# Kernel tuning notes

Hardware: AMD Instinct MI355X
Metric: run time of the kernel (lower is better)

The kernel has to match this reference:

```python
import jax, jax.numpy as jnp
import numpy as np
from jax import lax

N_NODES = 17
CONN = np.array([[15, 13], [13, 11], [16, 14], [14, 12], [11, 12], [5, 11], [6, 12],
                 [5, 6], [5, 7], [6, 8], [7, 9], [8, 10], [1, 2], [0, 1], [0, 2],
                 [1, 3], [2, 4], [3, 5], [4, 6]], dtype=np.int64)


def build_ahat():
    # PyG GCNConv norm: add self loops, deg = in-degree on target (col),
    # edge weight = deg^{-1/2}[src] * deg^{-1/2}[dst], aggregate src -> dst.
    src = np.concatenate([CONN[:, 0], np.arange(N_NODES)])
    dst = np.concatenate([CONN[:, 1], np.arange(N_NODES)])
    deg = np.zeros(N_NODES, dtype=np.float64)
    np.add.at(deg, dst, 1.0)
    dis = deg ** -0.5
    A = np.zeros((N_NODES, N_NODES), dtype=np.float64)
    np.add.at(A, (dst, src), dis[src] * dis[dst])
    return jnp.asarray(A, dtype=jnp.float32)

AHAT = build_ahat()  # (17, 17) normalized adjacency, directed as in source


def gcn_conv(h1, h2, W, b):
    # h1/h2: (B, T, 17, Cin). Only nodes 0..16 of the flattened cat(pose1, pose2)
    # batch -- i.e. pose1 sample 0 -- participate in message passing; all other
    # nodes only get their self-loop (weight 1) => plain linear.
    g1 = h1 @ W
    g2 = h2 @ W
    agg0 = jnp.einsum('ij,tjh->tih', AHAT, g1[0])  # (T, 17, H)
    g1 = g1.at[0].set(agg0)
    return g1 + b, g2 + b


def lstm_scan(x, Wih, Whh, bih, bhh, reverse=False):
    # x: (T, B, D). PyTorch gate order: i, f, g, o.
    B = x.shape[1]
    H = Whh.shape[1]
    xs = x[::-1] if reverse else x
    pre = xs @ Wih.T + (bih + bhh)  # (T, B, 4H), input part precomputed

    def step(carry, p):
        h, c = carry
        z = p + h @ Whh.T
        i, f, g, o = jnp.split(z, 4, axis=-1)
        c = jax.nn.sigmoid(f) * c + jax.nn.sigmoid(i) * jnp.tanh(g)
        h = jax.nn.sigmoid(o) * jnp.tanh(c)
        return (h, c), h

    init = (jnp.zeros((B, H), x.dtype), jnp.zeros((B, H), x.dtype))
    _, hs = lax.scan(step, init, pre)
    return hs[::-1] if reverse else hs  # time-ordered outputs (T, B, H)


def setup_inputs() -> dict:
    key = jax.random.key(0)
    ks = jax.random.split(key, 16)
    B, T, C_IN, H = 128, 256, 3, 128
    LH, NC = 256, 625
    D_LSTM = H * N_NODES  # 2176
    s = 0.05
    return {
        'pose1': jax.random.normal(ks[0], (B, T, N_NODES, C_IN), jnp.float32),
        'pose2': jax.random.normal(ks[1], (B, T, N_NODES, C_IN), jnp.float32),
        'W1': jax.random.normal(ks[2], (C_IN, H), jnp.float32) * s,
        'b1': jnp.zeros((H,), jnp.float32),
        'W2': jax.random.normal(ks[3], (H, H), jnp.float32) * s,
        'b2': jnp.zeros((H,), jnp.float32),
        'Wih_f': jax.random.normal(ks[4], (4 * LH, D_LSTM), jnp.float32) * s,
        'Whh_f': jax.random.normal(ks[5], (4 * LH, LH), jnp.float32) * s,
        'bih_f': jax.random.normal(ks[6], (4 * LH,), jnp.float32) * s,
        'bhh_f': jax.random.normal(ks[7], (4 * LH,), jnp.float32) * s,
        'Wih_b': jax.random.normal(ks[8], (4 * LH, D_LSTM), jnp.float32) * s,
        'Whh_b': jax.random.normal(ks[9], (4 * LH, LH), jnp.float32) * s,
        'bih_b': jax.random.normal(ks[10], (4 * LH,), jnp.float32) * s,
        'bhh_b': jax.random.normal(ks[11], (4 * LH,), jnp.float32) * s,
        'Wc': jax.random.normal(ks[12], (NC, 2 * LH), jnp.float32) * s,
        'bc': jnp.zeros((NC,), jnp.float32),
    }


def reference(pose1, pose2, W1, b1, W2, b2, Wih_f, Whh_f, bih_f, bhh_f,
              Wih_b, Whh_b, bih_b, bhh_b, Wc, bc):
    B, T = pose1.shape[:2]
    # GCN block (dropout is identity in eval mode)
    h1, h2 = gcn_conv(pose1, pose2, W1, b1)
    h1, h2 = jax.nn.relu(h1), jax.nn.relu(h2)
    h1, h2 = gcn_conv(h1, h2, W2, b2)
    # mean over the (pose1, pose2) pair, flatten node/channel dims
    feats = (0.5 * (h1 + h2)).reshape(B, T, -1)  # (B, T, 17*128)
    x = jnp.transpose(feats, (1, 0, 2))  # (T, B, D)
    hs_f = lstm_scan(x, Wih_f, Whh_f, bih_f, bhh_f, reverse=False)
    hs_b = lstm_scan(x, Wih_b, Whh_b, bih_b, bhh_b, reverse=True)
    last = jnp.concatenate([hs_f[-1], hs_b[-1]], axis=-1)  # (B, 512)
    feature_pool = jax.nn.relu(last)
    feature_cls = feature_pool @ Wc.T + bc
    return feature_pool, feature_cls
```

## Files before the change

### kernel.cpp

```cpp
#include <hip/hip_runtime.h>
#include <hip/hip_bf16.h>


#define TT 256
#define BB 128
#define NNODE 17
#define DD 2176
#define LHID 256
#define G4 1024
#define NCLS 625

typedef unsigned short u16t;

__device__ __constant__ int ESRC[19] = {15,13,16,14,11,5,6,5,5,6,7,8,1,0,0,1,2,3,4};
__device__ __constant__ int EDST[19] = {13,11,14,12,12,11,12,6,7,8,9,10,2,1,2,3,4,5,6};
__device__ __constant__ float DEGF[17] = {1,2,3,2,2,2,3,2,2,2,2,3,4,2,2,1,1};

__device__ inline float lo2f(unsigned u){ union{unsigned x; float f;} c; c.x = u << 16; return c.f; }
__device__ inline float hi2f(unsigned u){ union{unsigned x; float f;} c; c.x = u & 0xffff0000u; return c.f; }
__device__ inline u16t f2b(float f){
    __hip_bfloat16 h = __float2bfloat16(f);
    u16t s; __builtin_memcpy(&s, &h, 2); return s;
}
__device__ inline float b2f(u16t s){ union{unsigned x; float f;} c; c.x = ((unsigned)s) << 16; return c.f; }
__device__ inline unsigned pack2(float a, float b){
    return (unsigned)f2b(a) | ((unsigned)f2b(b) << 16);
}
__device__ inline float fsig(float x){ return __fdividef(1.f, 1.f + __expf(-x)); }
__device__ inline float ftanh(float x){ float e = __expf(2.f*x); return 1.f - __fdividef(2.f, e + 1.f); }
__device__ inline float sigm(float x){ return 1.f / (1.f + expf(-x)); }

typedef __attribute__((ext_vector_type(8))) short bf16x8;
typedef __attribute__((ext_vector_type(4))) float f32x4;
typedef __attribute__((ext_vector_type(4))) unsigned u32x4;

__device__ inline bf16x8 asB(u32x4 v){ bf16x8 r; __builtin_memcpy(&r, &v, 16); return r; }

__device__ inline void gload16(const void* g, void* l){
    __builtin_amdgcn_global_load_lds(
        (const __attribute__((address_space(1))) void*)g,
        (__attribute__((address_space(3))) void*)l, 16, 0, 0);
}

__global__ void k_w2t(const float* __restrict__ W2, __hip_bfloat16* __restrict__ W2Tb){
    int g = blockIdx.x * 256 + threadIdx.x;
    int k = g >> 7, n = g & 127;
    W2Tb[n * 128 + k] = __float2bfloat16(W2[g]);
}

__global__ void k_wb16(const float* __restrict__ W, u16t* __restrict__ Wb){
    int g = blockIdx.x * 256 + threadIdx.x;
    const float4 f0 = *(const float4*)(W + (size_t)g*8);
    const float4 f1 = *(const float4*)(W + (size_t)g*8 + 4);
    uint4 o;
    o.x = pack2(f0.x, f0.y); o.y = pack2(f0.z, f0.w);
    o.z = pack2(f1.x, f1.y); o.w = pack2(f1.z, f1.w);
    *(uint4*)(Wb + (size_t)g*8) = o;
}

__global__ void k_wfrag(const float* __restrict__ Whh, __hip_bfloat16* __restrict__ WTfrag){
    int g = blockIdx.x * 256 + threadIdx.x;
    int f = g >> 6, lane = g & 63;
    int w = f >> 5, kc = (f >> 2) & 7, nt = f & 3;
    int col = nt*256 + w*16 + (lane & 15);
    int k0  = kc*32 + (lane >> 4)*8;
    const float* src = Whh + (size_t)col * 256 + k0;
    float4 f0 = *(const float4*)src;
    float4 f1 = *(const float4*)(src + 4);
    uint4 o;
    o.x = pack2(f0.x, f0.y); o.y = pack2(f0.z, f0.w);
    o.z = pack2(f1.x, f1.y); o.w = pack2(f1.z, f1.w);
    *(uint4*)((char*)WTfrag + (size_t)g * 16) = o;
}

__global__ __launch_bounds__(512) void k_gcnfused(
    const float* __restrict__ pose1, const float* __restrict__ pose2,
    const float* __restrict__ W1, const float* __restrict__ b1,
    const float* __restrict__ b2, const __hip_bfloat16* __restrict__ W2Tb,
    __hip_bfloat16* __restrict__ feats)
{
    __shared__ u16t  Abuf[272][136];
    __shared__ u16t  BsmT[128][136];
    __shared__ float ps4[2][16][17][4];
    __shared__ float araw[17*128];
    __shared__ float araw2[17*128];
    __shared__ float As[289];

    const int tid = threadIdx.x;
    const int blk = blockIdx.x;
    const int t   = blk >> 3;
    const int bc  = blk & 7;

    for (int idx = tid; idx < 1632; idx += 512){
        int p_ = idx >= 816 ? 1 : 0;
        int r  = idx - p_ * 816;
        int bl = r / 51, i = r - bl * 51;
        int n = i / 3, c = i - n * 3;
        const float* src = p_ ? pose2 : pose1;
        ps4[p_][bl][n][c] = src[(size_t)((bc*16 + bl) * TT + t) * 51 + i];
    }
    {
        const uint4* src = (const uint4*)W2Tb;
        for (int r = 0; r < 2; ++r){
            int f0 = (tid + r * 512) * 16;
            int n = f0 >> 7, k0 = f0 & 127;
            uint4 v0 = src[(tid + r*512)*2 + 0];
            uint4 v1 = src[(tid + r*512)*2 + 1];
            *(uint4*)&BsmT[n][k0]     = v0;
            *(uint4*)&BsmT[n][k0 + 8] = v1;
        }
    }
    if (bc == 0 && tid < 289){
        int i = tid / 17, j = tid - (tid/17)*17;
        float a = (i == j) ? 1.0f / DEGF[i] : 0.0f;
        for (int e = 0; e < 19; ++e)
            if (EDST[e] == i && ESRC[e] == j)
                a += 1.0f / sqrtf(DEGF[i] * DEGF[j]);
        As[tid] = a;
    }

    const int h = tid & 127;
    const int q = tid >> 7;
    const float w10 = W1[h], w11 = W1[128 + h], w12 = W1[256 + h];
    const float b1h = b1[h];
    __syncthreads();

    float a2st[5];
    int nl[5], nv = 0;
    for (int s = 0; s < 5; ++s){ int n = q + 4*s; if (n < NNODE) nl[nv++] = n; }
    for (int s = 0; s < nv; ++s){
        int n = nl[s];
        for (int bl = 0; bl < 16; ++bl){
            float4 p1 = *(const float4*)&ps4[0][bl][n][0];
            float4 p2 = *(const float4*)&ps4[1][bl][n][0];
            float a1 = p1.x*w10 + p1.y*w11 + p1.z*w12;
            float a2 = p2.x*w10 + p2.y*w11 + p2.z*w12;
            if (bc == 0 && bl == 0){
                araw[n*128 + h] = a1;
                a2st[s] = a2;
            } else {
                float r1 = fmaxf(a1 + b1h, 0.f);
                float r2 = fmaxf(a2 + b1h, 0.f);
                Abuf[n*16 + bl][h] = f2b(0.5f*(r1 + r2));
            }
        }
    }
    __syncthreads();
    if (bc == 0){
        for (int s = 0; s < nv; ++s){
            int n = nl[s]; float a = 0.f;
            #pragma unroll
            for (int j = 0; j < NNODE; ++j) a += As[n*17 + j] * araw[j*128 + h];
            araw2[n*128 + h] = fmaxf(a + b1h, 0.f);
        }
    }
    __syncthreads();
    if (bc == 0){
        for (int s = 0; s < nv; ++s){
            int n = nl[s]; float a = 0.f;
            #pragma unroll
            for (int j = 0; j < NNODE; ++j) a += As[n*17 + j] * araw2[j*128 + h];
            float r2 = fmaxf(a2st[s] + b1h, 0.f);
            Abuf[n*16 + 0][h] = f2b(0.5f*(a + r2));
        }
    }
    __syncthreads();

    const int w = tid >> 6, l = tid & 63;
    const int l15 = l & 15, q8 = (l >> 4) * 8, q4 = (l >> 4) * 4;
    float bias[8];
    #pragma unroll
    for (int nt = 0; nt < 8; ++nt) bias[nt] = b2[nt*16 + l15];

    bf16x8 Bf[4][8];
    #pragma unroll
    for (int kc = 0; kc < 4; ++kc)
        #pragma unroll
        for (int nt = 0; nt < 8; ++nt)
            Bf[kc][nt] = *(const bf16x8*)&BsmT[nt*16 + l15][kc*32 + q8];

    u16t* Cb = (u16t*)feats;
    for (int mt = w; mt < NNODE; mt += 8){
        f32x4 acc[8];
        #pragma unroll
        for (int nt = 0; nt < 8; ++nt) acc[nt] = (f32x4){0.f,0.f,0.f,0.f};
        #pragma unroll
        for (int kc = 0; kc < 4; ++kc){
            bf16x8 a = *(const bf16x8*)&Abuf[mt*16 + l15][kc*32 + q8];
            #pragma unroll
            for (int nt = 0; nt < 8; ++nt)
                acc[nt] = __builtin_amdgcn_mfma_f32_16x16x32_bf16(a, Bf[kc][nt], acc[nt], 0,0,0);
        }
        #pragma unroll
        for (int nt = 0; nt < 8; ++nt)
            #pragma unroll
            for (int r = 0; r < 4; ++r){
                size_t row = (size_t)(blk*16 + q4 + r) * NNODE + mt;
                Cb[row*128 + nt*16 + l15] = f2b(acc[nt][r] + bias[nt]);
            }
    }
}

__global__ __launch_bounds__(256) void k_gemm_mfma(
    const __hip_bfloat16* __restrict__ A, const float* __restrict__ Bw,
    const u16t* __restrict__ Bb,
    const float* __restrict__ bi1, const float* __restrict__ bi2,
    u16t* __restrict__ pre2)
{
    __shared__ u16t Asm[128][32];
    __shared__ u16t Bsm[128][32];
    const int tid = threadIdx.x;
    const int w = tid >> 6;
    const int l = tid & 63;

    const int blk = blockIdx.x;
    const int xcd = blk & 7;
    const int i_  = blk >> 3;
    const int bx  = xcd * 32 + (i_ >> 3);
    const int by  = i_ & 7;

    const size_t m0 = (size_t)bx * 128;
    const int n0 = by * 128;
    const int mw = (w >> 1) * 64;
    const int nw = (w & 1) * 64;

    f32x4 acc[4][4];
    #pragma unroll
    for (int s = 0; s < 4; ++s)
        #pragma unroll
        for (int t_ = 0; t_ < 4; ++t_)
            acc[s][t_] = (f32x4){0.f, 0.f, 0.f, 0.f};

    const u16t* Ab = (const u16t*)A;
    const int arow = w*32 + (l>>2);
    const int akoff = (l&3)*8;
    const int brow = w*32 + (l>>1);
    const int bko  = (l&1)*16;
    const int fr = l & 15, fq = (l >> 4) * 8;

    for (int kt = 0; kt < DD; kt += 32){
        gload16(Ab + (m0 + arow)*DD + kt + akoff,      &Asm[arow][akoff]);
        gload16(Ab + (m0 + arow + 16)*DD + kt + akoff, &Asm[arow+16][akoff]);
        if (Bb){
            gload16(Bb + (size_t)(n0 + arow)*DD + kt + akoff,      &Bsm[arow][akoff]);
            gload16(Bb + (size_t)(n0 + arow + 16)*DD + kt + akoff, &Bsm[arow+16][akoff]);
        } else {
            const float* bp = Bw + (size_t)(n0 + brow)*DD + kt + bko;
            float4 f0 = *(const float4*)bp;
            float4 f1 = *(const float4*)(bp+4);
            float4 f2 = *(const float4*)(bp+8);
            float4 f3 = *(const float4*)(bp+12);
            uint4 o0, o1;
            o0.x = pack2(f0.x,f0.y); o0.y = pack2(f0.z,f0.w);
            o0.z = pack2(f1.x,f1.y); o0.w = pack2(f1.z,f1.w);
            o1.x = pack2(f2.x,f2.y); o1.y = pack2(f2.z,f2.w);
            o1.z = pack2(f3.x,f3.y); o1.w = pack2(f3.z,f3.w);
            *(uint4*)&Bsm[brow][bko]   = o0;
            *(uint4*)&Bsm[brow][bko+8] = o1;
        }
        __syncthreads();

        bf16x8 af[4], bf[4];
        #pragma unroll
        for (int s = 0; s < 4; ++s) af[s] = *(const bf16x8*)&Asm[mw + s*16 + fr][fq];
        #pragma unroll
        for (int t_ = 0; t_ < 4; ++t_) bf[t_] = *(const bf16x8*)&Bsm[nw + t_*16 + fr][fq];
        #pragma unroll
        for (int s = 0; s < 4; ++s)
            #pragma unroll
            for (int t_ = 0; t_ < 4; ++t_)
                acc[s][t_] = __builtin_amdgcn_mfma_f32_16x16x32_bf16(af[s], bf[t_], acc[s][t_], 0, 0, 0);
        __syncthreads();
    }

    const int cr = (l >> 4) * 4;
    const int cc = l & 15;
    const int tIdx = bx;
    #pragma unroll
    for (int t_ = 0; t_ < 4; ++t_){
        int col = n0 + nw + t_*16 + cc;
        float bias = bi1[col] + bi2[col];
        int gate = col >> 8;
        int j    = col & 255;
        size_t cbase = (size_t)tIdx*131072 + (size_t)(j>>4)*1024 + (size_t)(j&15)*4 + gate;
        #pragma unroll
        for (int s = 0; s < 4; ++s)
            #pragma unroll
            for (int r = 0; r < 4; ++r){
                int b = mw + s*16 + cr + r;
                pre2[cbase + (size_t)(b>>4)*16384 + ((b&15)>>2)*256 + (b&3)*64]
                    = f2b(acc[s][t_][r] + bias);
            }
    }
}

__global__ __launch_bounds__(256) void k_lstm_b(
    const __hip_bfloat16* __restrict__ feats255,
    const float* __restrict__ Wih_b,
    const float* __restrict__ bih_b, const float* __restrict__ bhh_b,
    float* __restrict__ h_b)
{
    __shared__ float fs[DD];
    const int tid = threadIdx.x;
    const int b = blockIdx.x;
    const unsigned* fbu = (const unsigned*)(feats255 + (size_t)b * DD);
    for (int i = tid; i < DD/2; i += 256){
        unsigned u = fbu[i];
        fs[2*i] = lo2f(u); fs[2*i+1] = hi2f(u);
    }
    __syncthreads();

    const int w = tid >> 6, lane = tid & 63;
    const int j = blockIdx.y * 4 + w;
    const float* Wi = Wih_b + (size_t)j * DD;
    const float* Wg = Wih_b + (size_t)(512 + j) * DD;
    const float* Wo = Wih_b + (size_t)(768 + j) * DD;
    float si = 0.f, sg = 0.f, so = 0.f;
    #pragma unroll 2
    for (int i = 0; i < 34; ++i){
        int k = lane + i*64;
        float f = fs[k];
        si += f * Wi[k]; sg += f * Wg[k]; so += f * Wo[k];
    }
    #pragma unroll
    for (int off = 32; off > 0; off >>= 1){
        si += __shfl_down(si, off);
        sg += __shfl_down(sg, off);
        so += __shfl_down(so, off);
    }
    if (lane == 0){
        float zi = si + bih_b[j]       + bhh_b[j];
        float zg = sg + bih_b[512 + j] + bhh_b[512 + j];
        float zo = so + bih_b[768 + j] + bhh_b[768 + j];
        float c = sigm(zi) * tanhf(zg);
        h_b[(size_t)b*LHID + j] = sigm(zo) * tanhf(c);
    }
}

__global__ __launch_bounds__(1024, 4) void k_lstm_f11(
    const u16t* __restrict__ pre2,
    const __hip_bfloat16* __restrict__ WTfrag,
    float* __restrict__ hout)
{
    __shared__ u16t Wl[65536];
    __shared__ __align__(16) float zbuf[256][4];
    __shared__ __align__(16) u16t hbuf[256];

    const int tid = threadIdx.x;
    const int w = tid >> 6, l = tid & 63;
    const int q = l >> 4, l15 = l & 15, q8 = q * 8;
    const int g = blockIdx.x;
    const u16t* wtf = (const u16t*)WTfrag;

    {
        const uint4* srcq = (const uint4*)wtf;
        uint4* dstq = (uint4*)Wl;
        for (int i = tid; i < 8192; i += 1024){
            int iw = i >> 9, fi = (i >> 6) & 7, il = i & 63;
            dstq[i] = srcq[(iw*32 + 24 + fi)*64 + il];
        }
    }
    if (tid < 256) hbuf[tid] = 0;

    u32x4 Bv[6][4];
    #pragma unroll
    for (int kc = 0; kc < 6; ++kc)
        #pragma unroll
        for (int nt = 0; nt < 4; ++nt){
            Bv[kc][nt] = *(const u32x4*)(wtf + (((size_t)(w*32 + kc*4 + nt))*64 + l)*8);
            asm volatile("" : "+v"(Bv[kc][nt]));
        }

    const int j = tid;
    float cst = 0.f;
    const size_t pj = (size_t)(g >> 4)*16384 + (size_t)((g & 15) >> 2)*256
                    + (size_t)(g & 3)*64 + (size_t)(j >> 4)*1024 + (size_t)(j & 15)*4;
    const u16t* pp = pre2 + pj;
    union { uint2 v; u16t s4[4]; } prc, prn;
    if (tid < 256) prc.v = *(const uint2*)pp;
    __syncthreads();

    #pragma unroll 1
    for (int t = 0; t < TT; ++t){
        if (tid < 256){
            int tn = (t + 1 < TT) ? t + 1 : t;
            prn.v = *(const uint2*)(pp + (size_t)tn*131072);
        }

        f32x4 acc[4];
        #pragma unroll
        for (int nt = 0; nt < 4; ++nt) acc[nt] = (f32x4){0.f,0.f,0.f,0.f};

        #pragma unroll
        for (int kc = 6; kc < 8; ++kc){
            bf16x8 ah = *(const bf16x8*)&hbuf[kc*32 + q8];
            #pragma unroll
            for (int nt = 0; nt < 4; ++nt){
                bf16x8 bL = *(const bf16x8*)&Wl[((w*8 + (kc-6)*4 + nt)*64 + l)*8];
                acc[nt] = __builtin_amdgcn_mfma_f32_16x16x32_bf16(ah, bL, acc[nt], 0,0,0);
            }
        }
        #pragma unroll
        for (int kc = 0; kc < 6; ++kc){
            bf16x8 ah = *(const bf16x8*)&hbuf[kc*32 + q8];
            #pragma unroll
            for (int nt = 0; nt < 4; ++nt)
                acc[nt] = __builtin_amdgcn_mfma_f32_16x16x32_bf16(ah, asB(Bv[kc][nt]), acc[nt], 0,0,0);
        }

        if (q == 0){
            float4 zq;
            zq.x = acc[0][0]; zq.y = acc[1][0]; zq.z = acc[2][0]; zq.w = acc[3][0];
            *(float4*)&zbuf[w*16 + l15][0] = zq;
        }
        __syncthreads();

        if (tid < 256){
            float4 z = *(const float4*)&zbuf[j][0];
            float zi = z.x + b2f(prc.s4[0]);
            float zf = z.y + b2f(prc.s4[1]);
            float zg = z.z + b2f(prc.s4[2]);
            float zo = z.w + b2f(prc.s4[3]);
            float cn = fsig(zf)*cst + fsig(zi)*ftanh(zg);
            cst = cn;
            float hh = fsig(zo)*ftanh(cn);
            if (t < TT - 1)
                hbuf[j] = f2b(hh);
            else
                hout[(size_t)g*LHID + j] = hh;
        }
        prc = prn;
        __syncthreads();
    }
}

__global__ __launch_bounds__(256) void k_head(
    const float* __restrict__ h_f, const float* __restrict__ h_b,
    const float* __restrict__ Wc, const float* __restrict__ bc,
    float* __restrict__ out)
{
    __shared__ float pool[512];
    const int b = blockIdx.x, tid = threadIdx.x;
    float p0 = fmaxf(h_f[(size_t)b*LHID + tid], 0.f);
    float p1 = fmaxf(h_b[(size_t)b*LHID + tid], 0.f);
    pool[tid] = p0; pool[256 + tid] = p1;
    out[(size_t)b*512 + tid]       = p0;
    out[(size_t)b*512 + 256 + tid] = p1;
    __syncthreads();
    for (int n = tid; n < NCLS; n += 256){
        float a = bc[n];
        const float* ww = Wc + (size_t)n * 512;
        #pragma unroll 4
        for (int k = 0; k < 512; k += 4){
            float4 wv = *(const float4*)(ww + k);
            a += pool[k]*wv.x + pool[k+1]*wv.y + pool[k+2]*wv.z + pool[k+3]*wv.w;
        }
        out[(size_t)BB*512 + (size_t)b*NCLS + n] = a;
    }
}

extern "C" void kernel_launch(void* const* d_in, const int* in_sizes, int n_in,
                              void* d_out, int out_size, void* d_ws, size_t ws_size,
                              hipStream_t stream) {
    const float* pose1 = (const float*)d_in[0];
    const float* pose2 = (const float*)d_in[1];
    const float* W1    = (const float*)d_in[2];
    const float* b1    = (const float*)d_in[3];
    const float* W2    = (const float*)d_in[4];
    const float* b2    = (const float*)d_in[5];
    const float* Wih_f = (const float*)d_in[6];
    const float* Whh_f = (const float*)d_in[7];
    const float* bih_f = (const float*)d_in[8];
    const float* bhh_f = (const float*)d_in[9];
    const float* Wih_b = (const float*)d_in[10];
    const float* bih_b = (const float*)d_in[12];
    const float* bhh_b = (const float*)d_in[13];
    const float* Wc    = (const float*)d_in[14];
    const float* bc    = (const float*)d_in[15];
    (void)in_sizes; (void)n_in; (void)out_size;
    float* out = (float*)d_out;
    char* ws = (char*)d_ws;

    __hip_bfloat16* WTfrag = (__hip_bfloat16*)(ws + 0);
    __hip_bfloat16* W2Tb   = (__hip_bfloat16*)(ws + 524288);
    float*          h_b    = (float*)(ws + 557056);
    float*          h_f    = (float*)(ws + 688128);
    __hip_bfloat16* feats  = (__hip_bfloat16*)(ws + 2097152);
    u16t*           pre2   = (u16t*)(ws + 144703488);

    const size_t BASE = 211812352, WBSZ = 4456448;
    const bool haveWb = (ws_size >= BASE + WBSZ);
    u16t* Wb16 = haveWb ? (u16t*)(ws + BASE) : (u16t*)nullptr;

    k_w2t     <<<64, 256, 0, stream>>>(W2, W2Tb);
    k_wfrag   <<<128, 256, 0, stream>>>(Whh_f, WTfrag);
    if (haveWb)
        k_wb16<<<1088, 256, 0, stream>>>(Wih_f, Wb16);
    k_gcnfused<<<2048, 512, 0, stream>>>(pose1, pose2, W1, b1, b2, W2Tb, feats);
    k_gemm_mfma<<<2048, 256, 0, stream>>>(feats, Wih_f, Wb16, bih_f, bhh_f, pre2);
    k_lstm_b  <<<dim3(128, 64), 256, 0, stream>>>(feats + (size_t)255*BB*DD, Wih_b, bih_b, bhh_b, h_b);
    k_lstm_f11<<<128, 1024, 0, stream>>>(pre2, WTfrag, h_f);
    k_head    <<<128, 256, 0, stream>>>(h_f, h_b, Wc, bc, out);
}
```

Baseline: 1.029 ms.

## Halve LSTM recurrence block to 512 threads, two tiles per wave in AGPRs

The forward LSTM recurrent kernel now runs with 512 threads instead of 1024, and each wave computes two 16-column gate tiles instead of one. The register-resident Whh fragments double and are pinned to accumulation registers (AGPRs) via an inline-asm constraint. Fewer waves means a cheaper per-step __syncthreads barrier and more MFMA work per wave between barriers. The cost is higher register pressure and less latency hiding per step.

```diff
diff --git a/kernel.cpp b/kernel.cpp
--- a/kernel.cpp
+++ b/kernel.cpp
@@ -337,7 +337,7 @@
     }
 }
 
-__global__ __launch_bounds__(1024, 4) void k_lstm_f11(
+__global__ __launch_bounds__(512, 2) void k_lstm_f16(
     const u16t* __restrict__ pre2,
     const __hip_bfloat16* __restrict__ WTfrag,
     float* __restrict__ hout)
@@ -355,21 +355,25 @@
     {
         const uint4* srcq = (const uint4*)wtf;
         uint4* dstq = (uint4*)Wl;
-        for (int i = tid; i < 8192; i += 1024){
+        for (int i = tid; i < 8192; i += 512){
             int iw = i >> 9, fi = (i >> 6) & 7, il = i & 63;
             dstq[i] = srcq[(iw*32 + 24 + fi)*64 + il];
         }
     }
     if (tid < 256) hbuf[tid] = 0;
 
-    u32x4 Bv[6][4];
+    u32x4 Ba[2][6][4];
     #pragma unroll
-    for (int kc = 0; kc < 6; ++kc)
-        #pragma unroll
-        for (int nt = 0; nt < 4; ++nt){
-            Bv[kc][nt] = *(const u32x4*)(wtf + (((size_t)(w*32 + kc*4 + nt))*64 + l)*8);
-            asm volatile("" : "+v"(Bv[kc][nt]));
-        }
+    for (int s = 0; s < 2; ++s){
+        const int wt = w + s*8;
+        #pragma unroll
+        for (int kc = 0; kc < 6; ++kc)
+            #pragma unroll
+            for (int nt = 0; nt < 4; ++nt){
+                Ba[s][kc][nt] = *(const u32x4*)(wtf + (((size_t)(wt*32 + kc*4 + nt))*64 + l)*8);
+                asm volatile("" : "+a"(Ba[s][kc][nt]));
+            }
+    }
 
     const int j = tid;
     float cst = 0.f;
@@ -387,31 +391,41 @@
             prn.v = *(const uint2*)(pp + (size_t)tn*131072);
         }
 
-        f32x4 acc[4];
-        #pragma unroll
-        for (int nt = 0; nt < 4; ++nt) acc[nt] = (f32x4){0.f,0.f,0.f,0.f};
+        f32x4 acc[2][4];
+        #pragma unroll
+        for (int s = 0; s < 2; ++s)
+            #pragma unroll
+            for (int nt = 0; nt < 4; ++nt) acc[s][nt] = (f32x4){0.f,0.f,0.f,0.f};
 
         #pragma unroll
         for (int kc = 6; kc < 8; ++kc){
             bf16x8 ah = *(const bf16x8*)&hbuf[kc*32 + q8];
             #pragma unroll
-            for (int nt = 0; nt < 4; ++nt){
-                bf16x8 bL = *(const bf16x8*)&Wl[((w*8 + (kc-6)*4 + nt)*64 + l)*8];
-                acc[nt] = __builtin_amdgcn_mfma_f32_16x16x32_bf16(ah, bL, acc[nt], 0,0,0);
+            for (int s = 0; s < 2; ++s){
+                const int wt = w + s*8;
+                #pragma unroll
+                for (int nt = 0; nt < 4; ++nt){
+                    bf16x8 bL = *(const bf16x8*)&Wl[((wt*8 + (kc-6)*4 + nt)*64 + l)*8];
+                    acc[s][nt] = __builtin_amdgcn_mfma_f32_16x16x32_bf16(ah, bL, acc[s][nt], 0,0,0);
+                }
             }
         }
         #pragma unroll
         for (int kc = 0; kc < 6; ++kc){
             bf16x8 ah = *(const bf16x8*)&hbuf[kc*32 + q8];
             #pragma unroll
-            for (int nt = 0; nt < 4; ++nt)
-                acc[nt] = __builtin_amdgcn_mfma_f32_16x16x32_bf16(ah, asB(Bv[kc][nt]), acc[nt], 0,0,0);
+            for (int s = 0; s < 2; ++s)
+                #pragma unroll
+                for (int nt = 0; nt < 4; ++nt)
+                    acc[s][nt] = __builtin_amdgcn_mfma_f32_16x16x32_bf16(ah, asB(Ba[s][kc][nt]), acc[s][nt], 0,0,0);
         }
 
         if (q == 0){
-            float4 zq;
-            zq.x = acc[0][0]; zq.y = acc[1][0]; zq.z = acc[2][0]; zq.w = acc[3][0];
-            *(float4*)&zbuf[w*16 + l15][0] = zq;
+            float4 z0, z1;
+            z0.x = acc[0][0][0]; z0.y = acc[0][1][0]; z0.z = acc[0][2][0]; z0.w = acc[0][3][0];
+            z1.x = acc[1][0][0]; z1.y = acc[1][1][0]; z1.z = acc[1][2][0]; z1.w = acc[1][3][0];
+            *(float4*)&zbuf[w*16 + l15][0]       = z0;
+            *(float4*)&zbuf[(w+8)*16 + l15][0]   = z1;
         }
         __syncthreads();
 
@@ -499,6 +513,6 @@
     k_gcnfused<<<2048, 512, 0, stream>>>(pose1, pose2, W1, b1, b2, W2Tb, feats);
     k_gemm_mfma<<<2048, 256, 0, stream>>>(feats, Wih_f, Wb16, bih_f, bhh_f, pre2);
     k_lstm_b  <<<dim3(128, 64), 256, 0, stream>>>(feats + (size_t)255*BB*DD, Wih_b, bih_b, bhh_b, h_b);
-    k_lstm_f11<<<128, 1024, 0, stream>>>(pre2, WTfrag, h_f);
+    k_lstm_f16<<<128, 512, 0, stream>>>(pre2, WTfrag, h_f);
     k_head    <<<128, 256, 0, stream>>>(h_f, h_b, Wc, bc, out);
 }
```

Result: faster. 970.6 us (median of 2 runs) (-5.7%).
